# Kernel optimization log

Measured on AMD Instinct MI355X. Metric: run time of the kernel, lower is better.

## Reference

```python
import jax, jax.numpy as jnp
import numpy as np

B, S, E, H = 4, 2048, 1024, 16
D = E // H          # head_dim = 64
FF = 3 * E          # feedforward_expansion = 3
EPS = 1.1920929e-07  # torch fp32 RMSNorm default eps (finfo.eps)


def rmsnorm(x, w):
    ms = jnp.mean(jnp.square(x), axis=-1, keepdims=True)
    return x * jax.lax.rsqrt(ms + EPS) * w


def setup_inputs() -> dict:
    key = jax.random.key(0)
    ks = jax.random.split(key, 12)
    s = 0.02
    return {
        "x": jax.random.normal(ks[0], (B, S, E), dtype=jnp.float32),
        "mask": jnp.ones((B, 1, 1, S), dtype=jnp.int32),
        "Wq": jax.random.normal(ks[1], (E, E), dtype=jnp.float32) * s,
        "bq": jnp.zeros((E,), dtype=jnp.float32),
        "Wkv": jax.random.normal(ks[2], (E, 2 * E), dtype=jnp.float32) * s,
        "bkv": jnp.zeros((2 * E,), dtype=jnp.float32),
        "Wo": jax.random.normal(ks[3], (E, E), dtype=jnp.float32) * s,
        "bo": jnp.zeros((E,), dtype=jnp.float32),
        "norm1_w": jnp.ones((E,), dtype=jnp.float32),
        "norm3_w": jnp.ones((E,), dtype=jnp.float32),
        "W1": jax.random.normal(ks[4], (E, FF), dtype=jnp.float32) * s,
        "b1": jnp.zeros((FF,), dtype=jnp.float32),
        "W2": jax.random.normal(ks[5], (FF, E), dtype=jnp.float32) * s,
        "b2": jnp.zeros((E,), dtype=jnp.float32),
    }


def attention(xn, mask, Wq, bq, Wkv, bkv, Wo, bo):
    q = xn @ Wq + bq                         # [B,S,E]
    kv = xn @ Wkv + bkv                      # [B,S,2E]
    k, v = jnp.split(kv, 2, axis=-1)
    q = q.reshape(B, S, H, D).transpose(0, 2, 1, 3)   # [B,H,S,D]
    k = k.reshape(B, S, H, D).transpose(0, 2, 1, 3)
    v = v.reshape(B, S, H, D).transpose(0, 2, 1, 3)
    scores = jnp.einsum("bhqd,bhkd->bhqk", q, k) / jnp.sqrt(jnp.float32(D))
    scores = jnp.where(mask == 0, -jnp.inf, scores)
    probs = jax.nn.softmax(scores, axis=-1)
    out = jnp.einsum("bhqk,bhkd->bhqd", probs, v)     # [B,H,S,D]
    out = out.transpose(0, 2, 1, 3).reshape(B, S, E)
    return out @ Wo + bo


def reference(x, mask, Wq, bq, Wkv, bkv, Wo, bo, norm1_w, norm3_w, W1, b1, W2, b2):
    # self-attention sublayer (pre-norm, residual; dropout = identity in eval)
    xn = rmsnorm(x, norm1_w)
    x = x + attention(xn, mask, Wq, bq, Wkv, bkv, Wo, bo)
    # feedforward sublayer: Linear -> exact GELU -> Linear
    xn = rmsnorm(x, norm3_w)
    h = jax.nn.gelu(xn @ W1 + b1, approximate=False)
    x = x + (h @ W2 + b2)
    return x
```

## Files before the change

kernel.cpp:

```cpp
#include <hip/hip_runtime.h>
#include <stdint.h>
#include <math.h>

typedef unsigned short u16;
typedef __attribute__((ext_vector_type(8))) short short8;
typedef __attribute__((ext_vector_type(4))) float f32x4;
typedef __attribute__((ext_vector_type(16))) float f32x16;
typedef __attribute__((ext_vector_type(4))) u16 u16x4;
typedef __attribute__((ext_vector_type(4))) uint32_t u32x4;
typedef __attribute__((ext_vector_type(2))) uint32_t u32x2;
typedef __attribute__((ext_vector_type(2))) int int2v;

#define DEV static __device__ __forceinline__

constexpr int Bb = 4, Ss = 2048, Ee = 1024, Hh = 16;
constexpr int MR = Bb * Ss;
constexpr int QKS = 2048;
constexpr float EPSf = 1.1920929e-07f;
constexpr float C1 = 0.125f * 1.44269504088896340736f;

DEV u16 f2bf(float f) {
  uint32_t u = __float_as_uint(f);
  u += 0x7FFFu + ((u >> 16) & 1u);
  return (u16)(u >> 16);
}

DEV uint32_t pkbf(float lo, float hi) {
  uint32_t r;
  asm("v_cvt_pk_bf16_f32 %0, %1, %2" : "=v"(r) : "v"(lo), "v"(hi));
  return r;
}

DEV float fexp2(float x) {
  float r;
  asm("v_exp_f32 %0, %1" : "=v"(r) : "v"(x));
  return r;
}
DEV float frcp(float x) {
  float r;
  asm("v_rcp_f32 %0, %1" : "=v"(r) : "v"(x));
  return r;
}

DEV float gelu_fast(float x) {
  const float inner = x * fmaf(x * x, 0.044715f, 1.0f);
  const float e = fexp2(inner * -2.3022082f);
  return x * frcp(1.0f + e);
}

typedef const __attribute__((address_space(1))) void* gas_cp;
typedef __attribute__((address_space(3))) void* las_p;

DEV void gload16(const void* g, void* l) {
  __builtin_amdgcn_global_load_lds((gas_cp)(uintptr_t)g,
                                   (las_p)(uint32_t)(uintptr_t)l, 16, 0, 0);
}

DEV float xchg32(float x, int lane) {
  int2v r = __builtin_amdgcn_permlane32_swap(__float_as_int(x), __float_as_int(x), false, false);
  return __int_as_float(lane < 32 ? r.x : r.y);
}

__global__ __launch_bounds__(256) void rmsnorm_kernel(const float* __restrict__ x,
                                                      const float* __restrict__ w,
                                                      u16* __restrict__ out) {
  const int row = blockIdx.x, tid = threadIdx.x;
  const float4 v = ((const float4*)(x + (size_t)row * Ee))[tid];
  float ss = v.x * v.x + v.y * v.y + v.z * v.z + v.w * v.w;
#pragma unroll
  for (int off = 1; off < 64; off <<= 1) ss += __shfl_xor(ss, off, 64);
  __shared__ float red[4];
  if ((tid & 63) == 0) red[tid >> 6] = ss;
  __syncthreads();
  const float total = red[0] + red[1] + red[2] + red[3];
  const float scale = rsqrtf(total * (1.0f / Ee) + EPSf);
  const float4 wv = ((const float4*)w)[tid];
  u16x4 o;
  o.x = f2bf(v.x * scale * wv.x);
  o.y = f2bf(v.y * scale * wv.y);
  o.z = f2bf(v.z * scale * wv.z);
  o.w = f2bf(v.w * scale * wv.w);
  ((u16x4*)(out + (size_t)row * Ee))[tid] = o;
}

__global__ __launch_bounds__(256) void transpose_cast_kernel(const float* __restrict__ in,
                                                             u16* __restrict__ out,
                                                             int R, int C) {
  __shared__ float t[32][33];
  const int c0 = blockIdx.x * 32, r0 = blockIdx.y * 32;
  const int tx = threadIdx.x, ty = threadIdx.y;
#pragma unroll
  for (int i = 0; i < 4; ++i)
    t[ty + i * 8][tx] = in[(size_t)(r0 + ty + i * 8) * C + c0 + tx];
  __syncthreads();
#pragma unroll
  for (int i = 0; i < 4; ++i) {
    const int cc = ty + i * 8;
    out[(size_t)(c0 + cc) * R + r0 + tx] = f2bf(t[tx][cc]);
  }
}

__global__ __launch_bounds__(256) void bias_concat_kernel(const float* __restrict__ bq,
                                                          const float* __restrict__ bkv,
                                                          float* __restrict__ o) {
  const int i = blockIdx.x * 256 + threadIdx.x;
  o[i] = (i < 1024) ? bq[i] : bkv[i - 1024];
}

template <int BN, int EPI>
__global__ __launch_bounds__(512) void gemm256(const u16* __restrict__ A,
                                               const u16* __restrict__ Bt,
                                               const float* __restrict__ bias,
                                               const float* __restrict__ resid,
                                               void* __restrict__ outp,
                                               int M, int N, int K) {
  constexpr int BM = 256, BK = 64;
  constexpr int NF = BN / 64;
  constexpr int ACH = 4;
  constexpr int BCH = BN / 64;
  constexpr int A_SZ = BM * BK;
  constexpr int B_SZ = BN * BK;
  constexpr int SLOT = A_SZ + B_SZ;
  __shared__ alignas(16) u16 lds[2 * SLOT];

  const int tid = threadIdx.x, lane = tid & 63, wave = tid >> 6;
  const int wr = wave >> 2, wc = wave & 3;
  const int nwg = (int)(gridDim.x * gridDim.y);
  int lin = (int)(blockIdx.y * gridDim.x + blockIdx.x);
  lin = (lin & 7) * (nwg >> 3) + (lin >> 3);
  const int bx = lin % (int)gridDim.x, by = lin / (int)gridDim.x;
  const int m0 = by * BM, n0 = bx * BN;
  const int l4 = lane >> 4, l15 = lane & 15, l7q = l15 & 7;

  const int strow = tid >> 3;
  const int scol = ((tid & 7) ^ (strow & 7)) * 8;
  const u16* asrc[ACH];
  const u16* bsrc[BCH];
#pragma unroll
  for (int c = 0; c < ACH; ++c) asrc[c] = A + (size_t)(m0 + c * 64 + strow) * K + scol;
#pragma unroll
  for (int c = 0; c < BCH; ++c) bsrc[c] = Bt + (size_t)(n0 + c * 64 + strow) * K + scol;
  const uint32_t ldto = (uint32_t)tid * 8;

  const int T = K >> 6;
  auto stage = [&](int t) {
    u16* base = &lds[(t & 1) * SLOT];
#pragma unroll
    for (int c = 0; c < ACH; ++c)
      gload16(asrc[c] + t * 64, base + c * 4096 + ldto);
#pragma unroll
    for (int c = 0; c < BCH; ++c)
      gload16(bsrc[c] + t * 64, base + A_SZ + c * 4096 + ldto);
  };

  f32x4 acc[8][NF];
#pragma unroll
  for (int i = 0; i < 8; ++i)
#pragma unroll
    for (int j = 0; j < NF; ++j) acc[i][j] = f32x4{0.f, 0.f, 0.f, 0.f};

  stage(0);
  for (int t = 0; t < T; ++t) {
    __builtin_amdgcn_s_barrier();
    __builtin_amdgcn_sched_barrier(0);
    if (t + 1 < T) stage(t + 1);
    __builtin_amdgcn_sched_barrier(0);
    if (t + 1 < T) {
      if constexpr (ACH + BCH == 8) asm volatile("s_waitcnt vmcnt(8)" ::: "memory");
      else                          asm volatile("s_waitcnt vmcnt(6)" ::: "memory");
    } else {
      asm volatile("s_waitcnt vmcnt(0)" ::: "memory");
    }
    __builtin_amdgcn_sched_barrier(0);

    const u16* sa = &lds[(t & 1) * SLOT];
    const u16* sb = sa + A_SZ;
#pragma unroll
    for (int kk = 0; kk < 2; ++kk) {
      short8 af[8], bf[NF];
#pragma unroll
      for (int i = 0; i < 8; ++i)
        af[i] = *(const short8*)&sa[(wr * 128 + i * 16 + l15) * 64 +
                                    (((kk * 4 + l4) ^ l7q) * 8)];
#pragma unroll
      for (int j = 0; j < NF; ++j)
        bf[j] = *(const short8*)&sb[(wc * (BN / 4) + j * 16 + l15) * 64 +
                                    (((kk * 4 + l4) ^ l7q) * 8)];
#pragma unroll
      for (int i = 0; i < 8; ++i)
#pragma unroll
        for (int j = 0; j < NF; ++j)
          acc[i][j] = __builtin_amdgcn_mfma_f32_16x16x32_bf16(af[i], bf[j],
                                                              acc[i][j], 0, 0, 0);
    }
  }

  const int rbase = m0 + wr * 128, cbase = n0 + wc * (BN / 4);
#pragma unroll
  for (int i = 0; i < 8; ++i) {
#pragma unroll
    for (int reg = 0; reg < 4; ++reg) {
      const int row = rbase + i * 16 + l4 * 4 + reg;
#pragma unroll
      for (int j = 0; j < NF; ++j) {
        const int col = cbase + j * 16 + l15;
        float v = acc[i][j][reg];
        if constexpr (EPI == 0) {
          v += bias[col];
          ((u16*)outp)[(size_t)row * N + col] = f2bf(v);
        } else if constexpr (EPI == 1) {
          v += bias[row];
          ((u16*)outp)[(size_t)row * N + col] = f2bf(v);
        } else if constexpr (EPI == 2) {
          v += bias[col] + resid[(size_t)row * N + col];
          ((float*)outp)[(size_t)row * N + col] = v;
        } else {
          v += bias[col];
          ((u16*)outp)[(size_t)row * N + col] = f2bf(gelu_fast(v));
        }
      }
    }
  }
}

__global__ __launch_bounds__(256, 4) void attn_kernel(const u16* __restrict__ qk,
                                                      const u16* __restrict__ vT,
                                                      u16* __restrict__ o) {
  __shared__ alignas(16) u16 Ks[2][64 * 64];
  __shared__ alignas(16) u16 Vs[2][64 * 64];

  const int tid = threadIdx.x, lane = tid & 63, wave = tid >> 6;
  const int bh = blockIdx.x, b = bh >> 4, h = bh & 15;
  const int q0 = blockIdx.y * 128;
  const int l31 = lane & 31, hi = lane >> 5, l7 = lane & 7;
  const int srow = lane >> 3;
  const int sw = ((lane & 7) ^ srow) * 8;

  const u16* qbase = qk + (size_t)(b * Ss + q0 + wave * 32 + l31) * QKS + h * 64;
  short8 qf[4];
#pragma unroll
  for (int ds = 0; ds < 4; ++ds)
    qf[ds] = *(const short8*)&qbase[ds * 16 + hi * 8];

  short8 ones;
#pragma unroll
  for (int i = 0; i < 8; ++i) ones[i] = (short)0x3F80;

  f32x16 accO[2];
  f32x16 accS;
#pragma unroll
  for (int dt = 0; dt < 2; ++dt)
#pragma unroll
    for (int r = 0; r < 16; ++r) accO[dt][r] = 0.f;
#pragma unroll
  for (int r = 0; r < 16; ++r) accS[r] = 0.f;
  float m = -INFINITY;

  const size_t krowbase = (size_t)(b * Ss) * QKS + 1024 + h * 64;
  const size_t vrowbase = (size_t)(h * 64) * MR + b * Ss;

  auto stage = [&](int buf, int kv0) {
#pragma unroll
    for (int c = 0; c < 4; ++c) {
      const int g = wave * 4 + c;
      if (g < 8) {
        const int r = g * 8 + srow;
        gload16(&qk[krowbase + (size_t)(kv0 + r) * QKS + sw], &Ks[buf][g * 512]);
      } else {
        const int gg = g - 8;
        const int dr = gg * 8 + srow;
        gload16(&vT[vrowbase + (size_t)dr * MR + kv0 + sw], &Vs[buf][gg * 512]);
      }
    }
  };

  stage(0, 0);
  constexpr int NT = Ss / 64;
  for (int t = 0; t < NT; ++t) {
    const int cur = t & 1;
    __syncthreads();
    if (t + 1 < NT) stage(cur ^ 1, (t + 1) * 64);

    f32x16 sct[2];
#pragma unroll
    for (int t2 = 0; t2 < 2; ++t2)
#pragma unroll
      for (int r = 0; r < 16; ++r) sct[t2][r] = 0.f;
#pragma unroll
    for (int ds = 0; ds < 4; ++ds) {
#pragma unroll
      for (int t2 = 0; t2 < 2; ++t2) {
        const short8 kf = *(const short8*)&Ks[cur][(t2 * 32 + l31) * 64 + (((ds * 2 + hi) ^ l7) * 8)];
        sct[t2] = __builtin_amdgcn_mfma_f32_32x32x16_bf16(kf, qf[ds], sct[t2], 0, 0, 0);
      }
    }

    float mx = fmaxf(sct[0][0], sct[0][1]);
#pragma unroll
    for (int r = 2; r < 16; r += 2) mx = fmaxf(fmaxf(mx, sct[0][r]), sct[0][r + 1]);
#pragma unroll
    for (int r = 0; r < 16; r += 2) mx = fmaxf(fmaxf(mx, sct[1][r]), sct[1][r + 1]);
    const float rowmax = fmaxf(mx, xchg32(mx, lane));

    if (__any(rowmax > m + 64.f)) {
      const float mnew = fmaxf(m, rowmax);
      const float corr = fexp2((m - mnew) * C1);
      m = mnew;
      accS[0] *= corr;
#pragma unroll
      for (int dt = 0; dt < 2; ++dt)
#pragma unroll
        for (int r = 0; r < 16; ++r) accO[dt][r] *= corr;
    }
    const float negmC = -m * C1;

#pragma unroll
    for (int t2 = 0; t2 < 2; ++t2) {
      float pv[16];
#pragma unroll
      for (int r = 0; r < 16; ++r) pv[r] = fexp2(fmaf(sct[t2][r], C1, negmC));
#pragma unroll
      for (int s2 = 0; s2 < 2; ++s2) {
        const uint32_t w0 = pkbf(pv[s2 * 8 + 0], pv[s2 * 8 + 1]);
        const uint32_t w1 = pkbf(pv[s2 * 8 + 2], pv[s2 * 8 + 3]);
        const uint32_t w2 = pkbf(pv[s2 * 8 + 4], pv[s2 * 8 + 5]);
        const uint32_t w3 = pkbf(pv[s2 * 8 + 6], pv[s2 * 8 + 7]);
        const int2v a = __builtin_amdgcn_permlane32_swap((int)w2, (int)w0, false, false);
        const int2v c = __builtin_amdgcn_permlane32_swap((int)w3, (int)w1, false, false);
        u32x4 fw; fw.x = (uint32_t)a.y; fw.y = (uint32_t)c.y; fw.z = (uint32_t)a.x; fw.w = (uint32_t)c.x;
        const short8 pf = *(const short8*)&fw;
        const int cb = (t2 * 2 + s2) * 2 + hi;
#pragma unroll
        for (int dt = 0; dt < 2; ++dt) {
          const short8 vf = *(const short8*)&Vs[cur][(dt * 32 + l31) * 64 + ((cb ^ l7) * 8)];
          accO[dt] = __builtin_amdgcn_mfma_f32_32x32x16_bf16(vf, pf, accO[dt], 0, 0, 0);
        }
        accS = __builtin_amdgcn_mfma_f32_32x32x16_bf16(ones, pf, accS, 0, 0, 0);
      }
    }
  }

  const float inv = 1.0f / accS[0];
  u16* obase = o + (size_t)(b * Ss + q0 + wave * 32 + l31) * Ee + h * 64;
#pragma unroll
  for (int dt = 0; dt < 2; ++dt) {
#pragma unroll
    for (int g4 = 0; g4 < 4; ++g4) {
      const int d0 = dt * 32 + g4 * 8 + 4 * hi;
      u32x2 w;
      w.x = pkbf(accO[dt][g4 * 4 + 0] * inv, accO[dt][g4 * 4 + 1] * inv);
      w.y = pkbf(accO[dt][g4 * 4 + 2] * inv, accO[dt][g4 * 4 + 3] * inv);
      *(u32x2*)&obase[d0] = w;
    }
  }
}

extern "C" void kernel_launch(void* const* d_in, const int* in_sizes, int n_in,
                              void* d_out, int out_size, void* d_ws, size_t ws_size,
                              hipStream_t stream) {
  const float* x   = (const float*)d_in[0];
  const float* Wq  = (const float*)d_in[2];
  const float* bq  = (const float*)d_in[3];
  const float* Wkv = (const float*)d_in[4];
  const float* bkv = (const float*)d_in[5];
  const float* Wo  = (const float*)d_in[6];
  const float* bo  = (const float*)d_in[7];
  const float* n1w = (const float*)d_in[8];
  const float* n3w = (const float*)d_in[9];
  const float* W1  = (const float*)d_in[10];
  const float* b1  = (const float*)d_in[11];
  const float* W2  = (const float*)d_in[12];
  const float* b2  = (const float*)d_in[13];
  float* out = (float*)d_out;

  char* p = (char*)d_ws;
  auto alloc = [&](size_t elems) { u16* r = (u16*)p; p += elems * sizeof(u16); return r; };
  u16* Wqt  = alloc((size_t)1024 * 1024);
  u16* Wkvt = alloc((size_t)2048 * 1024);
  u16* Wot  = alloc((size_t)1024 * 1024);
  u16* W1t  = alloc((size_t)3072 * 1024);
  u16* W2t  = alloc((size_t)1024 * 3072);
  u16* xn   = alloc((size_t)MR * 1024);
  u16* qkb  = alloc((size_t)MR * 2048);
  u16* vT   = alloc((size_t)1024 * MR);
  u16* ao   = alloc((size_t)MR * 1024);
  u16* hb   = alloc((size_t)MR * 3072);
  float* biasQK = (float*)p;

  const dim3 tb(32, 8);
  transpose_cast_kernel<<<dim3(1024 / 32, 1024 / 32), tb, 0, stream>>>(Wq, Wqt, 1024, 1024);
  transpose_cast_kernel<<<dim3(2048 / 32, 1024 / 32), tb, 0, stream>>>(Wkv, Wkvt, 1024, 2048);
  transpose_cast_kernel<<<dim3(1024 / 32, 1024 / 32), tb, 0, stream>>>(Wo, Wot, 1024, 1024);
  transpose_cast_kernel<<<dim3(3072 / 32, 1024 / 32), tb, 0, stream>>>(W1, W1t, 1024, 3072);
  transpose_cast_kernel<<<dim3(1024 / 32, 3072 / 32), tb, 0, stream>>>(W2, W2t, 3072, 1024);
  bias_concat_kernel<<<8, 256, 0, stream>>>(bq, bkv, biasQK);

  rmsnorm_kernel<<<MR, 256, 0, stream>>>(x, n1w, xn);

  gemm256<256, 0><<<dim3(2048 / 256, MR / 256), 512, 0, stream>>>(xn, Wqt, biasQK, nullptr, qkb, MR, 2048, 1024);
  gemm256<128, 1><<<dim3(MR / 128, 1024 / 256), 512, 0, stream>>>(Wkvt + (size_t)1024 * 1024, xn,
                                                                  bkv + 1024, nullptr, vT, 1024, MR, 1024);

  attn_kernel<<<dim3(Bb * Hh, Ss / 128), 256, 0, stream>>>(qkb, vT, ao);

  gemm256<128, 2><<<dim3(1024 / 128, MR / 256), 512, 0, stream>>>(ao, Wot, bo, x, out, MR, 1024, 1024);

  rmsnorm_kernel<<<MR, 256, 0, stream>>>(out, n3w, xn);

  gemm256<256, 3><<<dim3(3072 / 256, MR / 256), 512, 0, stream>>>(xn, W1t, b1, nullptr, hb, MR, 3072, 1024);
  gemm256<128, 2><<<dim3(1024 / 128, MR / 256), 512, 0, stream>>>(hb, W2t, b2, out, out, MR, 1024, 3072);
}
```

Baseline: 353.3 us.

## Prefetch two K-tiles ahead, split MFMA into phased groups, retile FFN up-proj

The GEMM main loop now issues global-to-LDS loads two stages ahead: it waits on the older stage, then launches the next load after compute. Compute is split into four phases with interleaved LDS reads, wave barriers and s_setprio raised around MFMA bursts, which lowers the number of live A-fragment registers. The W1 GEMM switches from BN=256 to BN=192, giving 16x32 workgroups instead of 12x32 for better CU fill. The extra barriers add sync overhead, and the vmcnt accounting has to match the new load counts, including the NLD=7 case.

Measured after the change: 361.9 us. 2.4% more time.

```diff
diff --git a/kernel.cpp b/kernel.cpp
--- a/kernel.cpp
+++ b/kernel.cpp
@@ -118,6 +118,7 @@
   constexpr int NF = BN / 64;
   constexpr int ACH = 4;
   constexpr int BCH = BN / 64;
+  constexpr int NLD = ACH + BCH;
   constexpr int A_SZ = BM * BK;
   constexpr int B_SZ = BN * BK;
   constexpr int SLOT = A_SZ + B_SZ;
@@ -160,39 +161,64 @@
     for (int j = 0; j < NF; ++j) acc[i][j] = f32x4{0.f, 0.f, 0.f, 0.f};
 
   stage(0);
+  stage(1);
   for (int t = 0; t < T; ++t) {
+    const u16* sa = &lds[(t & 1) * SLOT];
+    const u16* sb = sa + A_SZ;
+
+    __builtin_amdgcn_sched_barrier(0);
+    if (t + 1 < T) {
+      if constexpr (NLD == 8)      asm volatile("s_waitcnt vmcnt(8)" ::: "memory");
+      else if constexpr (NLD == 7) asm volatile("s_waitcnt vmcnt(7)" ::: "memory");
+      else                         asm volatile("s_waitcnt vmcnt(6)" ::: "memory");
+    } else {
+      asm volatile("s_waitcnt vmcnt(0)" ::: "memory");
+    }
+    __builtin_amdgcn_sched_barrier(0);
     __builtin_amdgcn_s_barrier();
     __builtin_amdgcn_sched_barrier(0);
-    if (t + 1 < T) stage(t + 1);
+
+    short8 bfr[NF];
+#define LDA(i, kk) (*(const short8*)&sa[(wr * 128 + (i) * 16 + l15) * 64 + \
+                                        ((((kk) * 4 + l4) ^ l7q) * 8)])
+#define LDB(j, kk) (*(const short8*)&sb[(wc * (BN / 4) + (j) * 16 + l15) * 64 + \
+                                        ((((kk) * 4 + l4) ^ l7q) * 8)])
+#define GPHASE(IH, KK, LOADB)                                                   \
+    do {                                                                        \
+      short8 af[4];                                                             \
+      if (LOADB) {                                                              \
+        _Pragma("unroll")                                                       \
+        for (int j = 0; j < NF; ++j) bfr[j] = LDB(j, KK);                       \
+      }                                                                         \
+      _Pragma("unroll")                                                         \
+      for (int i = 0; i < 4; ++i) af[i] = LDA((IH) * 4 + i, KK);                \
+      __builtin_amdgcn_sched_barrier(0);                                        \
+      __builtin_amdgcn_s_setprio(1);                                            \
+      _Pragma("unroll")                                                         \
+      for (int i = 0; i < 4; ++i)                                               \
+        _Pragma("unroll")                                                       \
+        for (int j = 0; j < NF; ++j)                                            \
+          acc[(IH) * 4 + i][j] = __builtin_amdgcn_mfma_f32_16x16x32_bf16(       \
+              af[i], bfr[j], acc[(IH) * 4 + i][j], 0, 0, 0);                    \
+      __builtin_amdgcn_s_setprio(0);                                            \
+      __builtin_amdgcn_sched_barrier(0);                                        \
+    } while (0)
+
+    GPHASE(0, 0, true);
+    __builtin_amdgcn_s_barrier();
+    GPHASE(1, 0, false);
+    __builtin_amdgcn_s_barrier();
+    GPHASE(0, 1, true);
+    __builtin_amdgcn_s_barrier();
+    GPHASE(1, 1, false);
+#undef GPHASE
+#undef LDA
+#undef LDB
+
     __builtin_amdgcn_sched_barrier(0);
-    if (t + 1 < T) {
-      if constexpr (ACH + BCH == 8) asm volatile("s_waitcnt vmcnt(8)" ::: "memory");
-      else                          asm volatile("s_waitcnt vmcnt(6)" ::: "memory");
-    } else {
-      asm volatile("s_waitcnt vmcnt(0)" ::: "memory");
-    }
+    __builtin_amdgcn_s_barrier();
     __builtin_amdgcn_sched_barrier(0);
-
-    const u16* sa = &lds[(t & 1) * SLOT];
-    const u16* sb = sa + A_SZ;
-#pragma unroll
-    for (int kk = 0; kk < 2; ++kk) {
-      short8 af[8], bf[NF];
-#pragma unroll
-      for (int i = 0; i < 8; ++i)
-        af[i] = *(const short8*)&sa[(wr * 128 + i * 16 + l15) * 64 +
-                                    (((kk * 4 + l4) ^ l7q) * 8)];
-#pragma unroll
-      for (int j = 0; j < NF; ++j)
-        bf[j] = *(const short8*)&sb[(wc * (BN / 4) + j * 16 + l15) * 64 +
-                                    (((kk * 4 + l4) ^ l7q) * 8)];
-#pragma unroll
-      for (int i = 0; i < 8; ++i)
-#pragma unroll
-        for (int j = 0; j < NF; ++j)
-          acc[i][j] = __builtin_amdgcn_mfma_f32_16x16x32_bf16(af[i], bf[j],
-                                                              acc[i][j], 0, 0, 0);
-    }
+    if (t + 2 < T) stage(t + 2);
   }
 
   const int rbase = m0 + wr * 128, cbase = n0 + wc * (BN / 4);
@@ -407,6 +433,6 @@
 
   rmsnorm_kernel<<<MR, 256, 0, stream>>>(out, n3w, xn);
 
-  gemm256<256, 3><<<dim3(3072 / 256, MR / 256), 512, 0, stream>>>(xn, W1t, b1, nullptr, hb, MR, 3072, 1024);
+  gemm256<192, 3><<<dim3(3072 / 192, MR / 256), 512, 0, stream>>>(xn, W1t, b1, nullptr, hb, MR, 3072, 1024);
   gemm256<128, 2><<<dim3(1024 / 128, MR / 256), 512, 0, stream>>>(hb, W2t, b2, out, out, MR, 1024, 3072);
 }
```
